# Optimization experiments

Hardware: AMD Instinct MI355X
Metric: run time of the kernel (lower is better)

## Reference

```python
import jax, jax.numpy as jnp
import numpy as np
import math

B, S, D, NH = 2, 2048, 1024, 16
DK = D // NH
E, TOPK, MOE_H, NSH = 8, 2, 1024, 2
SH_H = MOE_H * NSH
EPS = 1e-6


def setup_inputs() -> dict:
    key = jax.random.key(0)
    ks = jax.random.split(key, 24)
    p = lambda k, shape: jax.random.normal(k, shape, jnp.float32) * 0.02
    x = jax.random.normal(ks[0], (B, S, D), jnp.float32)
    # RoPE tables: freqs_cis = exp(i * t * theta^{-2j/dk}), passed as cos/sin
    inv = 1.0 / (10000.0 ** (np.arange(0, DK, 2, dtype=np.float32) / DK))
    ang = np.outer(np.arange(S, dtype=np.float32), inv)
    freqs_cos = jnp.asarray(np.cos(ang), jnp.float32)
    freqs_sin = jnp.asarray(np.sin(ang), jnp.float32)
    mask = jnp.triu(jnp.full((S, S), -1e9, jnp.float32), k=1)  # causal additive mask
    return {
        'x': x, 'freqs_cos': freqs_cos, 'freqs_sin': freqs_sin, 'mask': mask,
        'wq': p(ks[1], (D, D)), 'wk': p(ks[2], (D, D)),
        'wv': p(ks[3], (D, D)), 'wo': p(ks[4], (D, D)),
        'attn_norm_w': jnp.ones((D,), jnp.float32),
        'ffn_norm_w': jnp.ones((D,), jnp.float32),
        'gate_w': p(ks[5], (E, D)), 'gate_b': p(ks[6], (E,)),
        'w1': p(ks[7], (E, MOE_H, D)), 'b1': p(ks[8], (E, MOE_H)),
        'w2': p(ks[9], (E, D, MOE_H)), 'b2': p(ks[10], (E, D)),
        'w3': p(ks[11], (E, MOE_H, D)), 'b3': p(ks[12], (E, MOE_H)),
        'sg_w': p(ks[13], (SH_H, D)), 'su_w': p(ks[14], (SH_H, D)),
        'sd_w': p(ks[15], (D, SH_H)),
    }


def rmsnorm(x, w):
    f = x.astype(jnp.float32)
    y = f * jax.lax.rsqrt(jnp.mean(f * f, axis=-1, keepdims=True) + EPS)
    return y.astype(x.dtype) * w


def rope(t, cos, sin):
    # t: [b, s, h, dk]; pairs (t[2j], t[2j+1]) as complex, multiplied by e^{i ang}
    tr, ti = t[..., 0::2], t[..., 1::2]
    c, s = cos[None, :, None, :], sin[None, :, None, :]
    outr = tr * c - ti * s
    outi = tr * s + ti * c
    return jnp.stack([outr, outi], axis=-1).reshape(t.shape)


def reference(x, freqs_cos, freqs_sin, mask, wq, wk, wv, wo, attn_norm_w, ffn_norm_w,
              gate_w, gate_b, w1, b1, w2, b2, w3, b3, sg_w, su_w, sd_w):
    b, s, d = x.shape
    # --- attention with RoPE ---
    h = rmsnorm(x, attn_norm_w)
    q = (h @ wq.T).reshape(b, s, NH, DK)
    k = (h @ wk.T).reshape(b, s, NH, DK)
    v = (h @ wv.T).reshape(b, s, NH, DK)
    q = rope(q, freqs_cos, freqs_sin)
    k = rope(k, freqs_cos, freqs_sin)
    scale = 1.0 / math.sqrt(DK)
    q = q.transpose(0, 2, 1, 3)
    k = k.transpose(0, 2, 1, 3)
    v = v.transpose(0, 2, 1, 3)
    scores = jnp.einsum('bhqd,bhkd->bhqk', q, k) * scale + mask
    # NOTE: source divides by sqrt(d_k) a second time before softmax (faithful quirk)
    attn = jax.nn.softmax(scores * scale, axis=-1)
    o = jnp.einsum('bhqk,bhkd->bhqd', attn, v).transpose(0, 2, 1, 3).reshape(b, s, d)
    x = x + o @ wo.T
    # --- MoE FFN ---
    hf = rmsnorm(x, ffn_norm_w).reshape(-1, d)                 # [T, D]
    gscores = jax.nn.softmax(hf @ gate_w.T + gate_b, axis=-1)  # [T, E]
    _, idx = jax.lax.top_k(gscores, TOPK)                      # bias is None -> topk on scores
    weights = jnp.take_along_axis(gscores, idx, axis=1)        # original_scores gather
    wmask = (jax.nn.one_hot(idx, E, dtype=hf.dtype) * weights[..., None]).sum(1)  # [T, E]
    shared = (jax.nn.silu(hf @ sg_w.T) * (hf @ su_w.T)) @ sd_w.T
    a1 = jnp.einsum('td,ehd->teh', hf, w1) + b1
    a3 = jnp.einsum('td,ehd->teh', hf, w3) + b3
    eo = jnp.einsum('teh,edh->ted', jax.nn.silu(a1) * a3, w2) + b2  # [T, E, D]
    router = jnp.einsum('te,ted->td', wmask, eo)
    return x + (shared + router).reshape(x.shape)
```

## Files before the change

### kernel.cpp

```cpp
#include <hip/hip_runtime.h>


typedef unsigned short u16;
typedef __attribute__((ext_vector_type(8))) short bh8;
typedef __attribute__((ext_vector_type(4))) float fv4;
typedef __attribute__((ext_vector_type(4))) unsigned uv4;
typedef __attribute__((ext_vector_type(2))) int iv2;

#define LOG2E 1.4426950408889634f
#define MAX_TILES 71

__device__ __forceinline__ float b2f(u16 u) {
  return __builtin_bit_cast(float, ((unsigned)u) << 16);
}
__device__ __forceinline__ u16 f2b(float f) {
  unsigned x = __builtin_bit_cast(unsigned, f);
  return (u16)((x + 0x7fffu + ((x >> 16) & 1u)) >> 16);
}
__device__ __forceinline__ fv4 mfma16(bh8 a, bh8 b, fv4 c) {
  return __builtin_amdgcn_mfma_f32_16x16x32_bf16(a, b, c, 0, 0, 0);
}
__device__ __forceinline__ unsigned cvtpk(float lo, float hi) {
  unsigned r;
  asm("v_cvt_pk_bf16_f32 %0, %1, %2" : "=v"(r) : "v"(lo), "v"(hi));
  return r;
}

__device__ __forceinline__ int xcd_swizzle1d(int flat, int nwg) {
  int q = nwg >> 3, r = nwg & 7;
  int xcd = flat & 7, idx = flat >> 3;
  return (xcd < r ? xcd * (q + 1) : r * (q + 1) + (xcd - r) * q) + idx;
}

#define GLD16(g, l)                                                        \
  __builtin_amdgcn_global_load_lds(                                        \
      (const __attribute__((address_space(1))) void*)(g),                  \
      (__attribute__((address_space(3))) void*)(l), 16, 0, 0)

__device__ __forceinline__ bh8 lds_frag(const u16* base, int row, int b8) {
  int off = row * 128 + ((b8 * 16) ^ ((row & 7) << 4));
  return *(const bh8*)((const char*)base + off);
}

template <int MODE, int TM>
__device__ __forceinline__ void gemm_body(
    u16* AsB, u16* BsB, int bx, int by, const u16* __restrict__ A,
    const u16* __restrict__ B, int M, int N, int K, u16* __restrict__ Cb,
    float* __restrict__ Cf, const float* __restrict__ add1,
    const float* __restrict__ add2, const float* __restrict__ bias,
    const int* __restrict__ tmeta, const int* __restrict__ etok) {
  constexpr int MR = TM / 32;
  const int lane = threadIdx.x & 63;
  const int wid = threadIdx.x >> 6;
  const int wr = wid >> 1, wc = wid & 1;
  const int n0 = bx * 128;
  const int rr = lane >> 3;
  const int b8s = (lane & 7) ^ rr;
  const int ldA = (MODE == 6) ? M : K;

  int m0 = 0, e = 0, m0l = 0, cnt = 0, row0 = 0;
  const u16* Bp = B;
  if constexpr (MODE == 6 || MODE == 8) {
    int tile = by, half = 0;
    if constexpr (MODE == 6 && TM == 64) {
      tile = by >> 1;
      half = by & 1;
    }
    if (tile >= tmeta[0]) return;
    e = tmeta[16 + tile * 4];
    m0l = tmeta[17 + tile * 4];
    cnt = tmeta[18 + tile * 4];
    row0 = tmeta[19 + tile * 4] + half * 64;
    Bp = B + (size_t)e * N * K;
  } else {
    m0 = by * TM;
  }

  const u16* Arow[MR];
  const u16* Brow[4];
#pragma unroll
  for (int i = 0; i < MR; ++i) {
    int c = wid * MR + i;
    int row = c * 8 + rr;
    if constexpr (MODE == 8) {
      int li = m0l + row;
      li = li < cnt ? li : cnt - 1;
      int tok = etok[e * 4096 + li];
      Arow[i] = A + (size_t)tok * ldA + b8s * 8;
    } else if constexpr (MODE == 6) {
      Arow[i] = A + (size_t)(row0 + row) * ldA + b8s * 8;
    } else {
      Arow[i] = A + (size_t)(m0 + row) * ldA + b8s * 8;
    }
  }
#pragma unroll
  for (int i = 0; i < 4; ++i)
    Brow[i] = Bp + (size_t)(n0 + (wid * 4 + i) * 8 + rr) * K + b8s * 8;

  fv4 acc[MR][4] = {};
  const int nt = K >> 6;

#pragma unroll
  for (int i = 0; i < MR; ++i)
    GLD16(Arow[i], &AsB[(wid * MR + i) * 512]);
#pragma unroll
  for (int i = 0; i < 4; ++i)
    GLD16(Brow[i], &BsB[(wid * 4 + i) * 512]);

  for (int t = 0; t < nt; ++t) {
    const int cur = t & 1;
    u16* Asc = AsB + cur * (TM * 64);
    u16* Bsc = BsB + cur * (128 * 64);
    if (t + 1 < nt) {
      const int k0 = (t + 1) * 64;
      u16* Asn = AsB + (cur ^ 1) * (TM * 64);
      u16* Bsn = BsB + (cur ^ 1) * (128 * 64);
#pragma unroll
      for (int i = 0; i < MR; ++i)
        GLD16(Arow[i] + k0, &Asn[(wid * MR + i) * 512]);
#pragma unroll
      for (int i = 0; i < 4; ++i)
        GLD16(Brow[i] + k0, &Bsn[(wid * 4 + i) * 512]);
      if constexpr (MR == 4)
        asm volatile("s_waitcnt vmcnt(8)" ::: "memory");
      else
        asm volatile("s_waitcnt vmcnt(6)" ::: "memory");
    } else {
      asm volatile("s_waitcnt vmcnt(0)" ::: "memory");
    }
    __builtin_amdgcn_s_barrier();
    __builtin_amdgcn_sched_barrier(0);

#pragma unroll
    for (int ks = 0; ks < 2; ++ks) {
      int b8 = ks * 4 + (lane >> 4);
      bh8 af[MR], bf[4];
#pragma unroll
      for (int mi = 0; mi < MR; ++mi)
        af[mi] = lds_frag(Asc, wr * (16 * MR) + mi * 16 + (lane & 15), b8);
#pragma unroll
      for (int ni = 0; ni < 4; ++ni)
        bf[ni] = lds_frag(Bsc, wc * 64 + ni * 16 + (lane & 15), b8);
      __builtin_amdgcn_s_setprio(1);
#pragma unroll
      for (int mi = 0; mi < MR; ++mi)
#pragma unroll
        for (int ni = 0; ni < 4; ++ni)
          acc[mi][ni] = mfma16(af[mi], bf[ni], acc[mi][ni]);
      __builtin_amdgcn_s_setprio(0);
    }
    __builtin_amdgcn_sched_barrier(0);
    __builtin_amdgcn_s_barrier();
    __builtin_amdgcn_sched_barrier(0);
  }

  const int rbase = (MODE == 6 || MODE == 8) ? row0 : m0;
  const int r0b = rbase + wr * (16 * MR) + (lane >> 4) * 4;
  const int c0b = n0 + wc * 64 + (lane & 15);

  if constexpr (MODE == 7 || MODE == 8) {
    const int OUTN = N >> 1;
    const int colb = (n0 >> 1) + wc * 32;
    const float* bb1 = nullptr;
    const float* bb3 = nullptr;
    if constexpr (MODE == 8) {
      bb1 = add1 + (size_t)e * OUTN;
      bb3 = add2 + (size_t)e * OUTN;
    }
#pragma unroll
    for (int mi = 0; mi < MR; ++mi) {
#pragma unroll
      for (int ni = 0; ni < 2; ++ni) {
        int c = colb + ni * 16 + (lane & 15);
#pragma unroll
        for (int r = 0; r < 4; ++r) {
          int row = r0b + mi * 16 + r;
          float xg = acc[mi][ni][r];
          float yu = acc[mi][ni + 2][r];
          if constexpr (MODE == 8) {
            xg += bb1[c];
            yu += bb3[c];
          }
          float s = xg / (1.f + __expf(-xg));
          Cb[(size_t)row * OUTN + c] = f2b(s * yu);
        }
      }
    }
  } else if constexpr (MODE == 9) {
#pragma unroll
    for (int mi = 0; mi < MR; ++mi) {
#pragma unroll
      for (int r = 0; r < 4; ++r) {
        int row = r0b + mi * 16 + r;
        int g0 = tmeta[2 * row], g1 = tmeta[2 * row + 1];
        float w0 = bias[2 * row], w1 = bias[2 * row + 1];
        const u16* e0p = Cb + (size_t)g0 * 1024;
        const u16* e1p = Cb + (size_t)g1 * 1024;
#pragma unroll
        for (int ni = 0; ni < 4; ++ni) {
          int c = c0b + ni * 16;
          size_t idx = (size_t)row * N + c;
          Cf[idx] = add1[idx] + acc[mi][ni][r] + w0 * b2f(e0p[c]) +
                    w1 * b2f(e1p[c]);
        }
      }
    }
  } else {
    const float* bb = nullptr;
    if constexpr (MODE == 6) bb = bias + (size_t)e * N;
#pragma unroll
    for (int mi = 0; mi < MR; ++mi) {
#pragma unroll
      for (int ni = 0; ni < 4; ++ni) {
        int c = c0b + ni * 16;
#pragma unroll
        for (int r = 0; r < 4; ++r) {
          int row = r0b + mi * 16 + r;
          size_t idx = (size_t)row * N + c;
          float v = acc[mi][ni][r];
          if constexpr (MODE == 0) Cb[idx] = f2b(v);
          else if constexpr (MODE == 1) Cf[idx] = add1[idx] + v;
          else Cb[idx] = f2b(v + bb[c]);
        }
      }
    }
  }
}

template <int MODE, int TM = 128, int STILE = 0>
__global__ __launch_bounds__(256) void gemm_bt(
    const u16* __restrict__ A, const u16* __restrict__ B, int M, int N, int K,
    u16* __restrict__ Cb, float* __restrict__ Cf,
    const float* __restrict__ add1, const float* __restrict__ add2,
    const float* __restrict__ bias, const int* __restrict__ tmeta,
    const int* __restrict__ etok) {
  __shared__ u16 As[2][TM * 64];
  __shared__ u16 Bs[2][128 * 64];
  const int gx = gridDim.x;
  int flat = (int)blockIdx.y * gx + (int)blockIdx.x;
  flat = xcd_swizzle1d(flat, gx * (int)gridDim.y);
  int bx, by;
  if constexpr (STILE) {
    int SX = gx >> 2;
    int sidx = flat >> 5, within = flat & 31;
    int sy = sidx / SX, sx = sidx - sy * SX;
    by = sy * 8 + (within >> 2);
    bx = sx * 4 + (within & 3);
  } else {
    by = flat / gx;
    bx = flat - by * gx;
  }
  gemm_body<MODE, TM>(&As[0][0], &Bs[0][0], bx, by, A, B, M, N, K, Cb, Cf,
                      add1, add2, bias, tmeta, etok);
}

__global__ __launch_bounds__(256) void gemm_sgu_w13(
    const u16* __restrict__ hf, const u16* __restrict__ sgu_w,
    u16* __restrict__ hs, const u16* __restrict__ w13_w,
    u16* __restrict__ a13, const float* __restrict__ b1,
    const float* __restrict__ b3, const int* __restrict__ meta,
    const int* __restrict__ etok) {
  __shared__ u16 As[2][128 * 64];
  __shared__ u16 Bs[2][128 * 64];
  const int nwg = 1024 + 16 * MAX_TILES;
  int flat = xcd_swizzle1d((int)blockIdx.x, nwg);
  if (flat < 1024) {
    int sidx = flat >> 5, within = flat & 31;
    int sy = sidx >> 3, sx = sidx & 7;
    int by = sy * 8 + (within >> 2);
    int bx = sx * 4 + (within & 3);
    gemm_body<7, 128>(&As[0][0], &Bs[0][0], bx, by, hf, sgu_w, 4096, 4096,
                      1024, hs, nullptr, nullptr, nullptr, nullptr, nullptr,
                      nullptr);
  } else {
    int idx = flat - 1024;
    int by = idx >> 4, bx = idx & 15;
    gemm_body<8, 128>(&As[0][0], &Bs[0][0], bx, by, hf, w13_w, 4096, 2048,
                      1024, a13, nullptr, b1, b3, nullptr, meta, etok);
  }
}

__global__ __launch_bounds__(256) void rmsnorm_bf16(
    const float* __restrict__ x, const float* __restrict__ w,
    u16* __restrict__ out) {
  int t = blockIdx.x;
  const float* xr = x + (size_t)t * 1024;
  fv4 v = *(const fv4*)(xr + threadIdx.x * 4);
  float ss = v[0] * v[0] + v[1] * v[1] + v[2] * v[2] + v[3] * v[3];
#pragma unroll
  for (int off = 1; off < 64; off <<= 1) ss += __shfl_xor(ss, off);
  __shared__ float red[4];
  int lane = threadIdx.x & 63, wid = threadIdx.x >> 6;
  if (lane == 0) red[wid] = ss;
  __syncthreads();
  float inv = rsqrtf((red[0] + red[1] + red[2] + red[3]) * (1.0f / 1024.f) + 1e-6f);
  u16* op = out + (size_t)t * 1024 + threadIdx.x * 4;
  const float* wp = w + threadIdx.x * 4;
#pragma unroll
  for (int i = 0; i < 4; ++i) op[i] = f2b(v[i] * inv * wp[i]);
}

__global__ __launch_bounds__(256) void rope_repack(
    const u16* __restrict__ qkv, const float* __restrict__ fc,
    const float* __restrict__ fs, u16* __restrict__ qr, u16* __restrict__ kr,
    u16* __restrict__ vt, int S) {
  __shared__ u16 tile[64][65];
  const int s0 = blockIdx.x * 64;
  const int b = blockIdx.y;
  const int h0 = blockIdx.z * 4;
#pragma unroll 4
  for (int it = 0; it < 32; ++it) {
    int idx = threadIdx.x + it * 256;
    int tl = idx >> 7, rem = idx & 127;
    int h = h0 + (rem >> 5), i = rem & 31;
    int s = s0 + tl;
    float c = fc[s * 32 + i], sn = fs[s * 32 + i];
    size_t src = ((size_t)(b * S + s)) * 3072 + h * 64 + 2 * i;
    size_t dst = ((size_t)((b * 16 + h) * S + s)) * 64 + 2 * i;
    float a0 = b2f(qkv[src]), a1 = b2f(qkv[src + 1]);
    qr[dst] = f2b(a0 * c - a1 * sn);
    qr[dst + 1] = f2b(a0 * sn + a1 * c);
    float b0 = b2f(qkv[src + 1024]), b1 = b2f(qkv[src + 1025]);
    kr[dst] = f2b(b0 * c - b1 * sn);
    kr[dst + 1] = f2b(b0 * sn + b1 * c);
  }
  for (int hh = 0; hh < 4; ++hh) {
    int h = h0 + hh;
    __syncthreads();
    for (int cc = threadIdx.x; cc < 512; cc += 256) {
      int tl = cc >> 3, d8 = cc & 7;
      bh8 val = *(const bh8*)(qkv + ((size_t)(b * S + s0 + tl)) * 3072 + 2048 +
                              h * 64 + d8 * 8);
#pragma unroll
      for (int j = 0; j < 8; ++j) tile[tl][d8 * 8 + j] = (u16)val[j];
    }
    __syncthreads();
    for (int cc = threadIdx.x; cc < 512; cc += 256) {
      int d = cc >> 3, pg = cc & 7;
      int sbase = 16 * (pg >> 2) + 4 * (pg & 3);
      bh8 o;
#pragma unroll
      for (int j = 0; j < 8; ++j)
        o[j] = (short)tile[sbase + (j & 3) + ((j >> 2) << 5)][d];
      *(bh8*)(vt + ((size_t)((b * 16 + h) * 64 + d)) * S + s0 + pg * 8) = o;
    }
  }
}

__global__ __launch_bounds__(256) void attn_fwd(
    const u16* __restrict__ qr, const u16* __restrict__ kr,
    const u16* __restrict__ vt, u16* __restrict__ ob, int S, int NHc) {
  __shared__ u16 Ks[2][2][64 * 64];
  __shared__ u16 Vs[2][2][64 * 64];
  const int lane = threadIdx.x & 63;
  const int wid = threadIdx.x >> 6;
  const int g = lane >> 4;
  const int l15 = lane & 15;
  const int bh = blockIdx.x;
  const int ia = blockIdx.y;
  const int nq = S / 64;
  const int qa0 = ia * 64;
  const int qb0 = (nq - 1 - ia) * 64;
  const int b = bh / NHc, h = bh % NHc;
  const u16* qbase = qr + (size_t)bh * S * 64;
  const u16* kb = kr + (size_t)bh * S * 64;
  const u16* vb = vt + (size_t)bh * 64 * S;
  const float SC = 0.015625f * LOG2E;
  const int rr = lane >> 3;
  const int b8s = (lane & 7) ^ rr;

  bh8 ONES;
#pragma unroll
  for (int j = 0; j < 8; ++j) ONES[j] = (short)0x3f80;

  bh8 qfA[2], qfB[2];
  {
    const u16* qp = qbase + (size_t)(qa0 + wid * 16 + l15) * 64 + g * 8;
    qfA[0] = *(const bh8*)qp;
    qfA[1] = *(const bh8*)(qp + 32);
    qp = qbase + (size_t)(qb0 + wid * 16 + l15) * 64 + g * 8;
    qfB[0] = *(const bh8*)qp;
    qfB[1] = *(const bh8*)(qp + 32);
  }
  fv4 oaccA[4] = {}, oaccB[4] = {};
  fv4 lA = {}, lB = {};
  float mA = -1e30f, mB = -1e30f;
  const int nktB = nq - ia;
  const int nrounds = (nktB + 1) >> 1;

  auto stage = [&](int buf, int j0, int nsub) {
    for (int s = 0; s < nsub; ++s) {
#pragma unroll
      for (int i = 0; i < 2; ++i) {
        int c = wid * 2 + i;
        int row = c * 8 + rr;
        GLD16(kb + (size_t)(j0 + s * 64 + row) * 64 + b8s * 8,
              &Ks[buf][s][c * 512]);
        GLD16(vb + (size_t)row * S + j0 + s * 64 + b8s * 8,
              &Vs[buf][s][c * 512]);
      }
    }
  };
  stage(0, 0, nktB > 1 ? 2 : 1);

  auto process = [&](const bh8 (&kf)[2][4], const bh8 (&vf)[2][4], int j0,
                     int q0x, bh8* qf, fv4* oacc, float& mrow, fv4& lrowC) {
    const int q_my = q0x + wid * 16 + l15;
    fv4 st[4] = {};
    __builtin_amdgcn_s_setprio(1);
#pragma unroll
    for (int ks = 0; ks < 2; ++ks)
#pragma unroll
      for (int jt = 0; jt < 4; ++jt)
        st[jt] = mfma16(kf[ks][jt], qf[ks], st[jt]);
    __builtin_amdgcn_s_setprio(0);

    float sr[4][4];
    float mloc = -1e30f;
    const int jb = j0 + 4 * g;
    if (j0 + 63 > q0x + wid * 16) {
#pragma unroll
      for (int jt = 0; jt < 4; ++jt)
#pragma unroll
        for (int r = 0; r < 4; ++r) {
          int j = jb + jt * 16 + r;
          float s = (j <= q_my) ? st[jt][r] : -1e30f;
          sr[jt][r] = s;
          mloc = fmaxf(mloc, s);
        }
    } else {
#pragma unroll
      for (int jt = 0; jt < 4; ++jt)
#pragma unroll
        for (int r = 0; r < 4; ++r) {
          sr[jt][r] = st[jt][r];
          mloc = fmaxf(mloc, st[jt][r]);
        }
    }
    mloc = fmaxf(mloc, __shfl_xor(mloc, 16));
    mloc = fmaxf(mloc, __shfl_xor(mloc, 32));
    mloc *= SC;
    bool defer = __all(mloc <= mrow + 8.f);
    if (!defer) {
      float mnew = fmaxf(mrow, mloc);
      float sfac = exp2f(mrow - mnew);
      mrow = mnew;
      float sfC[4];
#pragma unroll
      for (int r = 0; r < 4; ++r) sfC[r] = __shfl(sfac, g * 4 + r);
#pragma unroll
      for (int dt = 0; dt < 4; ++dt)
#pragma unroll
        for (int r = 0; r < 4; ++r) oacc[dt][r] *= sfC[r];
#pragma unroll
      for (int r = 0; r < 4; ++r) lrowC[r] *= sfC[r];
    }
    float p[4][4];
#pragma unroll
    for (int jt = 0; jt < 4; ++jt)
#pragma unroll
      for (int r = 0; r < 4; ++r)
        p[jt][r] = exp2f(fmaf(sr[jt][r], SC, -mrow));

    __builtin_amdgcn_s_setprio(1);
    fv4 racc = {};
#pragma unroll
    for (int ks = 0; ks < 2; ++ks) {
      uv4 w;
      w[0] = cvtpk(p[ks][0], p[ks][1]);
      w[1] = cvtpk(p[ks][2], p[ks][3]);
      w[2] = cvtpk(p[ks + 2][0], p[ks + 2][1]);
      w[3] = cvtpk(p[ks + 2][2], p[ks + 2][3]);
      bh8 pa = __builtin_bit_cast(bh8, w);
      racc = mfma16(pa, ONES, racc);
#pragma unroll
      for (int dt = 0; dt < 4; ++dt)
        oacc[dt] = mfma16(pa, vf[ks][dt], oacc[dt]);
    }
    __builtin_amdgcn_s_setprio(0);
#pragma unroll
    for (int r = 0; r < 4; ++r) lrowC[r] += racc[r];
  };

  for (int rd = 0; rd < nrounds; ++rd) {
    __syncthreads();
    int rem = nktB - (rd + 1) * 2;
    if (rem > 0) stage((rd + 1) & 1, (rd + 1) * 128, rem > 1 ? 2 : 1);
#pragma unroll
    for (int s = 0; s < 2; ++s) {
      int kt = rd * 2 + s;
      if (kt >= nktB) break;
      const int j0 = kt * 64;
      const u16* Kc = Ks[rd & 1][s];
      const u16* Vc = Vs[rd & 1][s];
      bh8 kf[2][4], vf[2][4];
#pragma unroll
      for (int ks = 0; ks < 2; ++ks) {
        int b8 = ks * 4 + g;
#pragma unroll
        for (int jt = 0; jt < 4; ++jt)
          kf[ks][jt] = lds_frag(Kc, jt * 16 + l15, b8);
#pragma unroll
        for (int dt = 0; dt < 4; ++dt)
          vf[ks][dt] = lds_frag(Vc, dt * 16 + l15, b8);
      }
      process(kf, vf, j0, qb0, qfB, oaccB, mB, lB);
      if (kt <= ia) process(kf, vf, j0, qa0, qfA, oaccA, mA, lA);
    }
  }

  auto wout = [&](fv4* oacc, fv4 lrowC, int q0x) {
#pragma unroll
    for (int dt = 0; dt < 4; ++dt)
#pragma unroll
      for (int r = 0; r < 4; ++r) {
        int row = q0x + wid * 16 + g * 4 + r;
        int col = dt * 16 + l15;
        ob[((size_t)b * S + row) * 1024 + h * 64 + col] =
            f2b(oacc[dt][r] / lrowC[r]);
      }
  };
  wout(oaccA, lA, qa0);
  wout(oaccB, lB, qb0);
}

__global__ __launch_bounds__(256) void gate_topk(
    const float* __restrict__ x2, const float* __restrict__ nw,
    const float* __restrict__ gw, const float* __restrict__ gb,
    int* __restrict__ topk_e, float* __restrict__ topk_w,
    u16* __restrict__ hf) {
  int t = blockIdx.x * 4 + (threadIdx.x >> 6);
  int lane = threadIdx.x & 63;
  const float* xr = x2 + (size_t)t * 1024;
  float hv[16];
  float ss = 0.f;
#pragma unroll
  for (int i = 0; i < 4; ++i) {
    fv4 v = *(const fv4*)(xr + lane * 16 + i * 4);
#pragma unroll
    for (int j = 0; j < 4; ++j) {
      hv[i * 4 + j] = v[j];
      ss += v[j] * v[j];
    }
  }
#pragma unroll
  for (int off = 1; off < 64; off <<= 1) ss += __shfl_xor(ss, off);
  float inv = rsqrtf(ss * (1.0f / 1024.f) + 1e-6f);
  const fv4* nwp = (const fv4*)(nw + lane * 16);
#pragma unroll
  for (int i = 0; i < 4; ++i) {
    fv4 wv = nwp[i];
#pragma unroll
    for (int j = 0; j < 4; ++j) hv[i * 4 + j] *= inv * wv[j];
  }
  {
    bh8 o0, o1;
#pragma unroll
    for (int j = 0; j < 8; ++j) {
      o0[j] = (short)f2b(hv[j]);
      o1[j] = (short)f2b(hv[8 + j]);
    }
    u16* hp = hf + (size_t)t * 1024 + lane * 16;
    *(bh8*)hp = o0;
    *(bh8*)(hp + 8) = o1;
  }
  float logit[8];
#pragma unroll
  for (int e = 0; e < 8; ++e) {
    const fv4* wp = (const fv4*)(gw + (size_t)e * 1024 + lane * 16);
    float s = 0.f;
#pragma unroll
    for (int i = 0; i < 4; ++i) {
      fv4 wv = wp[i];
#pragma unroll
      for (int j = 0; j < 4; ++j) s += hv[i * 4 + j] * wv[j];
    }
    logit[e] = s;
  }
#pragma unroll
  for (int off = 1; off < 64; off <<= 1)
#pragma unroll
    for (int e = 0; e < 8; ++e) logit[e] += __shfl_xor(logit[e], off);
  if (lane == 0) {
#pragma unroll
    for (int e = 0; e < 8; ++e) logit[e] += gb[e];
    float mx = logit[0];
#pragma unroll
    for (int e = 1; e < 8; ++e) mx = fmaxf(mx, logit[e]);
    float pe[8], se = 0.f;
#pragma unroll
    for (int e = 0; e < 8; ++e) { pe[e] = __expf(logit[e] - mx); se += pe[e]; }
    float rs = 1.f / se;
#pragma unroll
    for (int e = 0; e < 8; ++e) pe[e] *= rs;
    int i0 = 0;
    float b0 = pe[0];
#pragma unroll
    for (int e = 1; e < 8; ++e)
      if (pe[e] > b0) { b0 = pe[e]; i0 = e; }
    int i1 = -1;
    float b1v = -1.f;
#pragma unroll
    for (int e = 0; e < 8; ++e)
      if (e != i0 && pe[e] > b1v) { b1v = pe[e]; i1 = e; }
    topk_e[2 * t] = i0;
    topk_e[2 * t + 1] = i1;
    topk_w[2 * t] = b0;
    topk_w[2 * t + 1] = b1v;
  }
}

__global__ __launch_bounds__(512) void route_tokens(
    const int* __restrict__ topk_e, int* __restrict__ pos_of,
    int* __restrict__ etok, int* __restrict__ meta, int* __restrict__ rowid,
    int T2) {
  __shared__ int scnt[8], sbase[8];
  const int e = threadIdx.x >> 6;
  const int lane = threadIdx.x & 63;
  int base = 0;
  for (int i0 = 0; i0 < T2; i0 += 128) {
    iv2 te = *(const iv2*)(topk_e + i0 + lane * 2);
    unsigned long long m0 = __ballot(te[0] == e);
    unsigned long long m1 = __ballot(te[1] == e);
    unsigned long long lt = (1ull << lane) - 1;
    int pre = __popcll(m0 & lt) + __popcll(m1 & lt);
    if (te[0] == e) {
      int pos = base + pre;
      etok[e * 4096 + pos] = (i0 >> 1) + lane;
      pos_of[i0 + lane * 2] = pos;
      ++pre;
    }
    if (te[1] == e) {
      int pos = base + pre;
      etok[e * 4096 + pos] = (i0 >> 1) + lane;
      pos_of[i0 + lane * 2 + 1] = pos;
    }
    base += __popcll(m0) + __popcll(m1);
  }
  if (lane == 0) scnt[e] = base;
  __syncthreads();
  if (threadIdx.x == 0) {
    int tt = 0, rb = 0;
#pragma unroll
    for (int e2 = 0; e2 < 8; ++e2) {
      sbase[e2] = rb;
      int c = scnt[e2];
      int nt = (c + 127) >> 7;
      for (int i = 0; i < nt; ++i) {
        meta[16 + tt * 4] = e2;
        meta[17 + tt * 4] = i * 128;
        meta[18 + tt * 4] = c;
        meta[19 + tt * 4] = rb + i * 128;
        ++tt;
      }
      rb += nt * 128;
    }
    meta[0] = tt;
  }
  __syncthreads();
  for (int i = threadIdx.x; i < T2; i += 512)
    rowid[i] = sbase[topk_e[i]] + pos_of[i];
}

__global__ __launch_bounds__(256) void f2b_convert(
    const float* __restrict__ src, u16* __restrict__ dst) {
  size_t i = ((size_t)blockIdx.x * 256 + threadIdx.x) * 8;
  fv4 a = *(const fv4*)(src + i);
  fv4 b = *(const fv4*)(src + i + 4);
  bh8 o;
#pragma unroll
  for (int j = 0; j < 4; ++j) o[j] = (short)f2b(a[j]);
#pragma unroll
  for (int j = 0; j < 4; ++j) o[4 + j] = (short)f2b(b[j]);
  *(bh8*)(dst + i) = o;
}

__global__ __launch_bounds__(256) void f2b_convert_ilv(
    const float* __restrict__ src, u16* __restrict__ dst, int half,
    int seg_shift) {
  size_t i = ((size_t)blockIdx.x * 256 + threadIdx.x) * 8;
  int r = (int)(i >> 10), col = (int)(i & 1023);
  int rl = r & ((1 << seg_shift) - 1), e = r >> seg_shift;
  int dstrow = (e << (seg_shift + 1)) + ((rl >> 5) << 6) + (rl & 31) +
               (half << 5);
  fv4 a = *(const fv4*)(src + i);
  fv4 b = *(const fv4*)(src + i + 4);
  bh8 o;
#pragma unroll
  for (int j = 0; j < 4; ++j) o[j] = (short)f2b(a[j]);
#pragma unroll
  for (int j = 0; j < 4; ++j) o[4 + j] = (short)f2b(b[j]);
  *(bh8*)(dst + (size_t)dstrow * 1024 + col) = o;
}

extern "C" void kernel_launch(void* const* d_in, const int* in_sizes, int n_in,
                              void* d_out, int out_size, void* d_ws,
                              size_t ws_size, hipStream_t stream) {
  (void)in_sizes; (void)n_in; (void)out_size; (void)ws_size;
  const int Sc = 2048, Dc = 1024, NHc = 16, Tc = 4096, SH = 2048;

  const float* x   = (const float*)d_in[0];
  const float* fc  = (const float*)d_in[1];
  const float* fs  = (const float*)d_in[2];
  const float* wq  = (const float*)d_in[4];
  const float* wk  = (const float*)d_in[5];
  const float* wv  = (const float*)d_in[6];
  const float* wo  = (const float*)d_in[7];
  const float* anw = (const float*)d_in[8];
  const float* fnw = (const float*)d_in[9];
  const float* gw  = (const float*)d_in[10];
  const float* gb  = (const float*)d_in[11];
  const float* w1  = (const float*)d_in[12];
  const float* b1  = (const float*)d_in[13];
  const float* w2  = (const float*)d_in[14];
  const float* b2  = (const float*)d_in[15];
  const float* w3  = (const float*)d_in[16];
  const float* b3  = (const float*)d_in[17];
  const float* sgw = (const float*)d_in[18];
  const float* suw = (const float*)d_in[19];
  const float* sdw = (const float*)d_in[20];
  float* out = (float*)d_out;

  char* base = (char*)d_ws;
  size_t off = 0;
  auto alloc = [&](size_t bytes) -> void* {
    void* p = base + off;
    off += (bytes + 255) & ~(size_t)255;
    return p;
  };
  u16* wqkv_b = (u16*)alloc(2ull * 3072 * 1024);
  u16* wo_b   = (u16*)alloc(2ull * 1024 * 1024);
  u16* sgu_b  = (u16*)alloc(2ull * 4096 * 1024);
  u16* sdw_b  = (u16*)alloc(2ull * 1024 * 2048);
  u16* w13_b  = (u16*)alloc(2ull * 8 * 2048 * 1024);
  u16* w2_b   = (u16*)alloc(2ull * 8 * 1024 * 1024);
  char* regA = (char*)alloc(2ull * Tc * 4096);
  char* regB = (char*)alloc(2ull * (size_t)MAX_TILES * 128 * 2048);
  float* x2  = (float*)alloc(4ull * Tc * Dc);
  u16* hs_b  = (u16*)alloc(2ull * Tc * SH);
  int* topk_e = (int*)alloc(2ull * Tc * 4);
  float* topk_w = (float*)alloc(2ull * Tc * 4);
  int* pos_of = (int*)alloc(2ull * Tc * 4);
  int* rowid = (int*)alloc(2ull * Tc * 4);
  int* etok = (int*)alloc(8ull * 4096 * 4);
  int* meta = (int*)alloc(512 * 4);

  u16* qkv_out = (u16*)regA;
  u16* eo_c    = (u16*)regA;
  u16* h_b  = (u16*)regB;
  u16* qr   = (u16*)regB;
  u16* kr   = (u16*)(regB + 2ull * Tc * Dc);
  u16* vt_  = (u16*)(regB + 4ull * Tc * Dc);
  u16* o_b  = (u16*)(regB + 6ull * Tc * Dc);
  u16* a13_c = (u16*)regB;
  u16* hf_b = wqkv_b;

  auto conv = [&](const float* s, u16* d, size_t n) {
    f2b_convert<<<dim3((unsigned)(n / 2048)), 256, 0, stream>>>(s, d);
  };
  conv(wq, wqkv_b, (size_t)Dc * Dc);
  conv(wk, wqkv_b + 1048576, (size_t)Dc * Dc);
  conv(wv, wqkv_b + 2097152, (size_t)Dc * Dc);
  conv(wo, wo_b, (size_t)Dc * Dc);
  conv(sdw, sdw_b, (size_t)Dc * SH);
  conv(w2, w2_b, 8ull * 1024 * 1024);
  f2b_convert_ilv<<<1024, 256, 0, stream>>>(sgw, sgu_b, 0, 11);
  f2b_convert_ilv<<<1024, 256, 0, stream>>>(suw, sgu_b, 1, 11);
  f2b_convert_ilv<<<4096, 256, 0, stream>>>(w1, w13_b, 0, 10);
  f2b_convert_ilv<<<4096, 256, 0, stream>>>(w3, w13_b, 1, 10);

  rmsnorm_bf16<<<Tc, 256, 0, stream>>>(x, anw, h_b);
  gemm_bt<0, 128, 1><<<dim3(3072 / 128, Tc / 128), 256, 0, stream>>>(
      h_b, wqkv_b, Tc, 3072, Dc, qkv_out, nullptr, nullptr, nullptr, nullptr,
      nullptr, nullptr);
  rope_repack<<<dim3(Sc / 64, 2, 4), 256, 0, stream>>>(qkv_out, fc, fs, qr, kr,
                                                       vt_, Sc);
  attn_fwd<<<dim3(2 * NHc, Sc / 128), 256, 0, stream>>>(qr, kr, vt_, o_b, Sc,
                                                        NHc);
  gemm_bt<1, 64, 1><<<dim3(Dc / 128, Tc / 64), 256, 0, stream>>>(
      o_b, wo_b, Tc, Dc, Dc, nullptr, x2, x, nullptr, nullptr, nullptr,
      nullptr);

  gate_topk<<<Tc / 4, 256, 0, stream>>>(x2, fnw, gw, gb, topk_e, topk_w,
                                        hf_b);
  route_tokens<<<1, 512, 0, stream>>>(topk_e, pos_of, etok, meta, rowid,
                                      2 * Tc);

  gemm_sgu_w13<<<dim3(1024 + 16 * MAX_TILES), 256, 0, stream>>>(
      hf_b, sgu_b, hs_b, w13_b, a13_c, b1, b3, meta, etok);

  gemm_bt<6, 64><<<dim3(Dc / 128, 2 * MAX_TILES), 256, 0, stream>>>(
      a13_c, w2_b, 1024, Dc, 1024, eo_c, nullptr, nullptr, nullptr,
      b2, meta, etok);

  gemm_bt<9, 64, 1><<<dim3(Dc / 128, Tc / 64), 256, 0, stream>>>(
      hs_b, sdw_b, Tc, Dc, SH, eo_c, out, x2, nullptr, topk_w, rowid,
      nullptr);
}
```

Measured before the change: 398.3 us.

## Use 8 waves per GEMM block with a 2x4 wave grid

Every GEMM kernel now launches 512 threads (8 waves) instead of 256. Waves are arranged 2x4, so each wave computes half as many N columns (2 fragments instead of 4), and global-to-LDS copies are split across more waves. For the SwiGLU modes the B fragment columns are remapped so each wave still holds matching gate/up pairs. This is meant to raise latency hiding and occupancy per CU, at the cost of less register reuse per wave and more LDS fragment reads relative to MFMA work.

```diff
diff --git a/kernel.cpp b/kernel.cpp
--- a/kernel.cpp
+++ b/kernel.cpp
@@ -50,10 +50,12 @@
     const float* __restrict__ add2, const float* __restrict__ bias,
     const int* __restrict__ tmeta, const int* __restrict__ etok) {
   constexpr int MR = TM / 32;
+  constexpr int ACL = TM / 64;
   const int lane = threadIdx.x & 63;
   const int wid = threadIdx.x >> 6;
-  const int wr = wid >> 1, wc = wid & 1;
+  const int wr = wid >> 2, wc = wid & 3;
   const int n0 = bx * 128;
+  const int l15 = lane & 15;
   const int rr = lane >> 3;
   const int b8s = (lane & 7) ^ rr;
   const int ldA = (MODE == 6) ? M : K;
@@ -76,11 +78,11 @@
     m0 = by * TM;
   }
 
-  const u16* Arow[MR];
-  const u16* Brow[4];
-#pragma unroll
-  for (int i = 0; i < MR; ++i) {
-    int c = wid * MR + i;
+  const u16* Arow[ACL];
+  const u16* Brow[2];
+#pragma unroll
+  for (int i = 0; i < ACL; ++i) {
+    int c = wid * ACL + i;
     int row = c * 8 + rr;
     if constexpr (MODE == 8) {
       int li = m0l + row;
@@ -94,18 +96,18 @@
     }
   }
 #pragma unroll
-  for (int i = 0; i < 4; ++i)
-    Brow[i] = Bp + (size_t)(n0 + (wid * 4 + i) * 8 + rr) * K + b8s * 8;
-
-  fv4 acc[MR][4] = {};
+  for (int i = 0; i < 2; ++i)
+    Brow[i] = Bp + (size_t)(n0 + (wid * 2 + i) * 8 + rr) * K + b8s * 8;
+
+  fv4 acc[MR][2] = {};
   const int nt = K >> 6;
 
 #pragma unroll
-  for (int i = 0; i < MR; ++i)
-    GLD16(Arow[i], &AsB[(wid * MR + i) * 512]);
-#pragma unroll
-  for (int i = 0; i < 4; ++i)
-    GLD16(Brow[i], &BsB[(wid * 4 + i) * 512]);
+  for (int i = 0; i < ACL; ++i)
+    GLD16(Arow[i], &AsB[(wid * ACL + i) * 512]);
+#pragma unroll
+  for (int i = 0; i < 2; ++i)
+    GLD16(Brow[i], &BsB[(wid * 2 + i) * 512]);
 
   for (int t = 0; t < nt; ++t) {
     const int cur = t & 1;
@@ -116,15 +118,15 @@
       u16* Asn = AsB + (cur ^ 1) * (TM * 64);
       u16* Bsn = BsB + (cur ^ 1) * (128 * 64);
 #pragma unroll
-      for (int i = 0; i < MR; ++i)
-        GLD16(Arow[i] + k0, &Asn[(wid * MR + i) * 512]);
-#pragma unroll
-      for (int i = 0; i < 4; ++i)
-        GLD16(Brow[i] + k0, &Bsn[(wid * 4 + i) * 512]);
-      if constexpr (MR == 4)
-        asm volatile("s_waitcnt vmcnt(8)" ::: "memory");
+      for (int i = 0; i < ACL; ++i)
+        GLD16(Arow[i] + k0, &Asn[(wid * ACL + i) * 512]);
+#pragma unroll
+      for (int i = 0; i < 2; ++i)
+        GLD16(Brow[i] + k0, &Bsn[(wid * 2 + i) * 512]);
+      if constexpr (ACL == 2)
+        asm volatile("s_waitcnt vmcnt(4)" ::: "memory");
       else
-        asm volatile("s_waitcnt vmcnt(6)" ::: "memory");
+        asm volatile("s_waitcnt vmcnt(3)" ::: "memory");
     } else {
       asm volatile("s_waitcnt vmcnt(0)" ::: "memory");
     }
@@ -134,18 +136,24 @@
 #pragma unroll
     for (int ks = 0; ks < 2; ++ks) {
       int b8 = ks * 4 + (lane >> 4);
-      bh8 af[MR], bf[4];
+      bh8 af[MR], bf[2];
 #pragma unroll
       for (int mi = 0; mi < MR; ++mi)
-        af[mi] = lds_frag(Asc, wr * (16 * MR) + mi * 16 + (lane & 15), b8);
-#pragma unroll
-      for (int ni = 0; ni < 4; ++ni)
-        bf[ni] = lds_frag(Bsc, wc * 64 + ni * 16 + (lane & 15), b8);
+        af[mi] = lds_frag(Asc, wr * (16 * MR) + mi * 16 + l15, b8);
+      if constexpr (MODE == 7 || MODE == 8) {
+        int col0 = (wc >> 1) * 64 + (wc & 1) * 16;
+        bf[0] = lds_frag(Bsc, col0 + l15, b8);
+        bf[1] = lds_frag(Bsc, col0 + 32 + l15, b8);
+      } else {
+#pragma unroll
+        for (int ni = 0; ni < 2; ++ni)
+          bf[ni] = lds_frag(Bsc, wc * 32 + ni * 16 + l15, b8);
+      }
       __builtin_amdgcn_s_setprio(1);
 #pragma unroll
       for (int mi = 0; mi < MR; ++mi)
 #pragma unroll
-        for (int ni = 0; ni < 4; ++ni)
+        for (int ni = 0; ni < 2; ++ni)
           acc[mi][ni] = mfma16(af[mi], bf[ni], acc[mi][ni]);
       __builtin_amdgcn_s_setprio(0);
     }
@@ -156,11 +164,10 @@
 
   const int rbase = (MODE == 6 || MODE == 8) ? row0 : m0;
   const int r0b = rbase + wr * (16 * MR) + (lane >> 4) * 4;
-  const int c0b = n0 + wc * 64 + (lane & 15);
 
   if constexpr (MODE == 7 || MODE == 8) {
     const int OUTN = N >> 1;
-    const int colb = (n0 >> 1) + wc * 32;
+    const int c = (n0 >> 1) + (wc >> 1) * 32 + (wc & 1) * 16 + l15;
     const float* bb1 = nullptr;
     const float* bb3 = nullptr;
     if constexpr (MODE == 8) {
@@ -170,23 +177,20 @@
 #pragma unroll
     for (int mi = 0; mi < MR; ++mi) {
 #pragma unroll
-      for (int ni = 0; ni < 2; ++ni) {
-        int c = colb + ni * 16 + (lane & 15);
-#pragma unroll
-        for (int r = 0; r < 4; ++r) {
-          int row = r0b + mi * 16 + r;
-          float xg = acc[mi][ni][r];
-          float yu = acc[mi][ni + 2][r];
-          if constexpr (MODE == 8) {
-            xg += bb1[c];
-            yu += bb3[c];
-          }
-          float s = xg / (1.f + __expf(-xg));
-          Cb[(size_t)row * OUTN + c] = f2b(s * yu);
+      for (int r = 0; r < 4; ++r) {
+        int row = r0b + mi * 16 + r;
+        float xg = acc[mi][0][r];
+        float yu = acc[mi][1][r];
+        if constexpr (MODE == 8) {
+          xg += bb1[c];
+          yu += bb3[c];
         }
+        float s = xg / (1.f + __expf(-xg));
+        Cb[(size_t)row * OUTN + c] = f2b(s * yu);
       }
     }
   } else if constexpr (MODE == 9) {
+    const int c0b = n0 + wc * 32 + l15;
 #pragma unroll
     for (int mi = 0; mi < MR; ++mi) {
 #pragma unroll
@@ -197,7 +201,7 @@
         const u16* e0p = Cb + (size_t)g0 * 1024;
         const u16* e1p = Cb + (size_t)g1 * 1024;
 #pragma unroll
-        for (int ni = 0; ni < 4; ++ni) {
+        for (int ni = 0; ni < 2; ++ni) {
           int c = c0b + ni * 16;
           size_t idx = (size_t)row * N + c;
           Cf[idx] = add1[idx] + acc[mi][ni][r] + w0 * b2f(e0p[c]) +
@@ -206,12 +210,13 @@
       }
     }
   } else {
+    const int c0b = n0 + wc * 32 + l15;
     const float* bb = nullptr;
     if constexpr (MODE == 6) bb = bias + (size_t)e * N;
 #pragma unroll
     for (int mi = 0; mi < MR; ++mi) {
 #pragma unroll
-      for (int ni = 0; ni < 4; ++ni) {
+      for (int ni = 0; ni < 2; ++ni) {
         int c = c0b + ni * 16;
 #pragma unroll
         for (int r = 0; r < 4; ++r) {
@@ -228,7 +233,7 @@
 }
 
 template <int MODE, int TM = 128, int STILE = 0>
-__global__ __launch_bounds__(256) void gemm_bt(
+__global__ __launch_bounds__(512) void gemm_bt(
     const u16* __restrict__ A, const u16* __restrict__ B, int M, int N, int K,
     u16* __restrict__ Cb, float* __restrict__ Cf,
     const float* __restrict__ add1, const float* __restrict__ add2,
@@ -254,7 +259,7 @@
                       add1, add2, bias, tmeta, etok);
 }
 
-__global__ __launch_bounds__(256) void gemm_sgu_w13(
+__global__ __launch_bounds__(512) void gemm_sgu_w13(
     const u16* __restrict__ hf, const u16* __restrict__ sgu_w,
     u16* __restrict__ hs, const u16* __restrict__ w13_w,
     u16* __restrict__ a13, const float* __restrict__ b1,
@@ -770,14 +775,14 @@
   f2b_convert_ilv<<<4096, 256, 0, stream>>>(w3, w13_b, 1, 10);
 
   rmsnorm_bf16<<<Tc, 256, 0, stream>>>(x, anw, h_b);
-  gemm_bt<0, 128, 1><<<dim3(3072 / 128, Tc / 128), 256, 0, stream>>>(
+  gemm_bt<0, 128, 1><<<dim3(3072 / 128, Tc / 128), 512, 0, stream>>>(
       h_b, wqkv_b, Tc, 3072, Dc, qkv_out, nullptr, nullptr, nullptr, nullptr,
       nullptr, nullptr);
   rope_repack<<<dim3(Sc / 64, 2, 4), 256, 0, stream>>>(qkv_out, fc, fs, qr, kr,
                                                        vt_, Sc);
   attn_fwd<<<dim3(2 * NHc, Sc / 128), 256, 0, stream>>>(qr, kr, vt_, o_b, Sc,
                                                         NHc);
-  gemm_bt<1, 64, 1><<<dim3(Dc / 128, Tc / 64), 256, 0, stream>>>(
+  gemm_bt<1, 64, 1><<<dim3(Dc / 128, Tc / 64), 512, 0, stream>>>(
       o_b, wo_b, Tc, Dc, Dc, nullptr, x2, x, nullptr, nullptr, nullptr,
       nullptr);
 
@@ -786,14 +791,14 @@
   route_tokens<<<1, 512, 0, stream>>>(topk_e, pos_of, etok, meta, rowid,
                                       2 * Tc);
 
-  gemm_sgu_w13<<<dim3(1024 + 16 * MAX_TILES), 256, 0, stream>>>(
+  gemm_sgu_w13<<<dim3(1024 + 16 * MAX_TILES), 512, 0, stream>>>(
       hf_b, sgu_b, hs_b, w13_b, a13_c, b1, b3, meta, etok);
 
-  gemm_bt<6, 64><<<dim3(Dc / 128, 2 * MAX_TILES), 256, 0, stream>>>(
+  gemm_bt<6, 64><<<dim3(Dc / 128, 2 * MAX_TILES), 512, 0, stream>>>(
       a13_c, w2_b, 1024, Dc, 1024, eo_c, nullptr, nullptr, nullptr,
       b2, meta, etok);
 
-  gemm_bt<9, 64, 1><<<dim3(Dc / 128, Tc / 64), 256, 0, stream>>>(
+  gemm_bt<9, 64, 1><<<dim3(Dc / 128, Tc / 64), 512, 0, stream>>>(
       hs_b, sdw_b, Tc, Dc, SH, eo_c, out, x2, nullptr, topk_w, rowid,
       nullptr);
 }
```

New measurement: 384.4 us. -3.5%, faster.
